# Kernel optimization log

Hardware: AMD Instinct MI355X
Metric: run time of the kernel (lower is better)

Reference implementation:

```python
import jax, jax.numpy as jnp
import numpy as np

B, T, N, H, RC, APT = 8, 32, 144, 16, 16, 10
HN = H * N          # 2304
RCN = RC * N        # 2304
NUM_LAYERS = 2


def _lstm_scan(x, Wih, Whh, bih, bhh):
    # x: [B, D, T] -> hidden states [B, HN, T]; matches torch.nn.LSTMCell math
    b = x.shape[0]
    hd = Whh.shape[1]
    xs = jnp.moveaxis(x, 2, 0)  # [T, B, D]

    def step(carry, xt):
        h, c = carry
        g = xt @ Wih.T + bih + h @ Whh.T + bhh  # [B, 4*HN]
        i, f, gg, o = jnp.split(g, 4, axis=1)
        c = jax.nn.sigmoid(f) * c + jax.nn.sigmoid(i) * jnp.tanh(gg)
        h = jax.nn.sigmoid(o) * jnp.tanh(c)
        return (h, c), h

    init = (jnp.zeros((b, hd), x.dtype), jnp.zeros((b, hd), x.dtype))
    _, hs = jax.lax.scan(step, init, xs)  # [T, B, HN]
    return jnp.moveaxis(hs, 0, 2)  # [B, HN, T]


def _graph_conv(x, A, Wg, bg):
    # x: [B, H, N, T]; diffusion order 2 over one adaptive support, then 1x1 conv
    x1 = jnp.einsum('bcvt,vw->bcwt', x, A)
    x2 = jnp.einsum('bcvt,vw->bcwt', x1, A)
    h = jnp.concatenate([x, x1, x2], axis=1)  # [B, 3H, N, T]
    return jnp.einsum('bcnt,oc->bont', h, Wg) + bg[None, :, None, None]


def _bn(x, g, b, eps=1e-5):
    # BatchNorm2d in training mode (batch statistics over N,H,W)
    m = x.mean(axis=(0, 2, 3), keepdims=True)
    v = x.var(axis=(0, 2, 3), keepdims=True)
    return g[None, :, None, None] * (x - m) * jax.lax.rsqrt(v + eps) + b[None, :, None, None]


def _forward(input_tensor, mask, input_tensor_bw, mask_bw, y, ymask,
             ws, bs, wc, bc, nodevec1, nodevec2,
             Wih_fw, Whh_fw, bih_fw, bhh_fw,
             Wih_bw, Whh_bw, bih_bw, bhh_bw,
             Wg, bg, gamma, beta,
             W_end1, b_end1, W_end2, b_end2,
             W_lo, b_lo, W_f1, b_f1, W_f2, b_f2):

    def feat(inp, m):
        # stack->transpose(2,3) then two 1x1 convs (in_channels=1 each), summed
        f1 = jnp.swapaxes(inp, 1, 2)[:, None]  # [B,1,N,T]
        f2 = jnp.swapaxes(m, 1, 2)[:, None]
        return (ws[None, :, None, None] * f1 + bs[None, :, None, None]
                + wc[None, :, None, None] * f2 + bc[None, :, None, None])

    x = feat(input_tensor, mask)          # [B, RC, N, T]
    x_bw = feat(input_tensor_bw, mask_bw)
    adp = jax.nn.softmax(jax.nn.relu(nodevec1 @ nodevec2), axis=1)  # [N, N]

    outputs = None
    for l in range(NUM_LAYERS):
        t_l = x.shape[3]
        hs = _lstm_scan(x.reshape(B, -1, t_l), Wih_fw[l], Whh_fw[l], bih_fw[l], bhh_fw[l])
        if l == 0:
            hs_bw = _lstm_scan(x_bw.reshape(B, -1, t_l), Wih_bw, Whh_bw, bih_bw, bhh_bw)
            hs = (hs + hs_bw[..., ::-1]) / 2.0
        gcn_in = jnp.tanh(hs.reshape(B, H, N, t_l))
        go = _graph_conv(gcn_in, adp, Wg[l], bg[l])  # [B, RC, N, t_l]
        outputs = go if outputs is None else go + outputs[..., -t_l:]
        x = _bn(go[..., ::2], gamma[l], beta[l])  # halve time dim

    out = jnp.einsum('bcnt,oc->bont', outputs, W_end1) + b_end1[None, :, None, None]
    out = jnp.einsum('bcnt,oc->bont', out, W_end2) + b_end2[None, :, None, None]
    out = jnp.einsum('bcnt,t->bcn', out, W_lo[0]) + b_lo[0]  # linear over time, squeeze
    out = jnp.concatenate([out, y, ymask], axis=-1)  # [B, T, 3N]
    out = out @ W_f1.T + b_f1
    out = out @ W_f2.T + b_f2
    return out  # [B, T, N]


def setup_inputs() -> dict:
    key = jax.random.key(0)
    ks = iter(jax.random.split(key, 48))
    nrm = lambda shape, s=0.05: jax.random.normal(next(ks), shape, dtype=jnp.float32) * s
    rnd = lambda shape: jax.random.uniform(next(ks), shape, dtype=jnp.float32)
    d = {}
    for name in ['input_tensor', 'mask', 'input_tensor_bw', 'mask_bw', 'y', 'ymask']:
        d[name] = rnd((B, T, N))
    d['ws'] = nrm((RC,), 0.2); d['bs'] = nrm((RC,))
    d['wc'] = nrm((RC,), 0.2); d['bc'] = nrm((RC,))
    d['nodevec1'] = nrm((N, APT), 1.0); d['nodevec2'] = nrm((APT, N), 1.0)
    d['Wih_fw'] = nrm((NUM_LAYERS, 4 * HN, RCN), 0.02)
    d['Whh_fw'] = nrm((NUM_LAYERS, 4 * HN, HN), 0.02)
    d['bih_fw'] = nrm((NUM_LAYERS, 4 * HN)); d['bhh_fw'] = nrm((NUM_LAYERS, 4 * HN))
    d['Wih_bw'] = nrm((4 * HN, RCN), 0.02); d['Whh_bw'] = nrm((4 * HN, HN), 0.02)
    d['bih_bw'] = nrm((4 * HN,)); d['bhh_bw'] = nrm((4 * HN,))
    d['Wg'] = nrm((NUM_LAYERS, RC, 3 * H), 0.1); d['bg'] = nrm((NUM_LAYERS, RC))
    d['gamma'] = jnp.ones((NUM_LAYERS, RC), jnp.float32)
    d['beta'] = jnp.zeros((NUM_LAYERS, RC), jnp.float32)
    d['W_end1'] = nrm((H, RC), 0.1); d['b_end1'] = nrm((H,))
    d['W_end2'] = nrm((T, H), 0.1); d['b_end2'] = nrm((T,))
    d['W_lo'] = nrm((1, T // 2), 0.1); d['b_lo'] = nrm((1,))
    d['W_f1'] = nrm((128, 3 * N), 0.05); d['b_f1'] = nrm((128,))
    d['W_f2'] = nrm((N, 128), 0.05); d['b_f2'] = nrm((N,))
    return d


def reference(input_tensor, mask, input_tensor_bw, mask_bw, y, ymask,
              ws, bs, wc, bc, nodevec1, nodevec2,
              Wih_fw, Whh_fw, bih_fw, bhh_fw,
              Wih_bw, Whh_bw, bih_bw, bhh_bw,
              Wg, bg, gamma, beta,
              W_end1, b_end1, W_end2, b_end2,
              W_lo, b_lo, W_f1, b_f1, W_f2, b_f2):
    return _forward(input_tensor, mask, input_tensor_bw, mask_bw, y, ymask,
                    ws, bs, wc, bc, nodevec1, nodevec2,
                    Wih_fw, Whh_fw, bih_fw, bhh_fw,
                    Wih_bw, Whh_bw, bih_bw, bhh_bw,
                    Wg, bg, gamma, beta,
                    W_end1, b_end1, W_end2, b_end2,
                    W_lo, b_lo, W_f1, b_f1, W_f2, b_f2)
```

## Files before the change

### kernel.cpp

```cpp
#include <hip/hip_runtime.h>
#include <cstdint>
#include <cstddef>

#define HN_ 2304
#define G4_ 9216

typedef __attribute__((ext_vector_type(8))) short v8s;
typedef __attribute__((ext_vector_type(4))) float v4f;

__device__ __forceinline__ unsigned short f2bf(float x) {
  union { float f; unsigned int i; } v; v.f = x;
  unsigned int r = (v.i + 0x7fffu + ((v.i >> 16) & 1u)) >> 16;
  return (unsigned short)r;
}

__global__ __launch_bounds__(256) void adp_kernel(const float* __restrict__ nv1,
                                                  const float* __restrict__ nv2,
                                                  float* __restrict__ adp) {
  int i = blockIdx.x;
  int j = threadIdx.x;
  __shared__ float sm[256];
  float r = 0.f, v = -1e30f;
  if (j < 144) {
    for (int k = 0; k < 10; ++k) r += nv1[i * 10 + k] * nv2[k * 144 + j];
    r = fmaxf(r, 0.f);
    v = r;
  }
  sm[j] = v; __syncthreads();
  for (int s = 128; s > 0; s >>= 1) { if (j < s) sm[j] = fmaxf(sm[j], sm[j + s]); __syncthreads(); }
  float mx = sm[0]; __syncthreads();
  float e = (j < 144) ? expf(r - mx) : 0.f;
  sm[j] = e; __syncthreads();
  for (int s = 128; s > 0; s >>= 1) { if (j < s) sm[j] += sm[j + s]; __syncthreads(); }
  float sum = sm[0];
  if (j < 144) adp[i * 144 + j] = e / sum;
}

__global__ __launch_bounds__(256)
void eff_weights(const float* __restrict__ WihF, const float* __restrict__ WihB,
                 const float* __restrict__ bihF, const float* __restrict__ bhhF,
                 const float* __restrict__ bihB, const float* __restrict__ bhhB,
                 const float* __restrict__ ws, const float* __restrict__ bs,
                 const float* __restrict__ wc, const float* __restrict__ bc,
                 unsigned short* __restrict__ Wpk, float* __restrict__ beff) {
  const int r = blockIdx.x, dir = blockIdx.y;
  const float* W = dir ? WihB : WihF;
  __shared__ float red[256];
  const int n = threadIdx.x;
  float spb = 0.f;
  if (n < 144) {
    float sws = 0.f, swc = 0.f;
    #pragma unroll
    for (int c = 0; c < 16; ++c) {
      float w = W[(size_t)r * HN_ + c * 144 + n];
      sws += w * ws[c];
      swc += w * wc[c];
      spb += w * (bs[c] + bc[c]);
    }
    const int rm = r % 2304;
    const int g = r / 2304;
    const int nt = rm >> 2, col = (rm & 3) * 4 + g;
    unsigned short* outp = Wpk + (size_t)dir * 2654208;
    int k = n;
    outp[((size_t)(nt * 9 + (k >> 5)) * 64 + ((k >> 3) & 3) * 16 + col) * 8 + (k & 7)] = f2bf(sws);
    k = 144 + n;
    outp[((size_t)(nt * 9 + (k >> 5)) * 64 + ((k >> 3) & 3) * 16 + col) * 8 + (k & 7)] = f2bf(swc);
  }
  red[n] = spb; __syncthreads();
  for (int s = 128; s > 0; s >>= 1) { if (n < s) red[n] += red[n + s]; __syncthreads(); }
  if (n == 0) {
    const float* bih = dir ? bihB : bihF;
    const float* bhh = dir ? bhhB : bhhF;
    beff[dir * G4_ + r] = red[0] + bih[r] + bhh[r];
  }
}

__global__ void build_acat_frag(const float* __restrict__ inF, const float* __restrict__ mF,
                                const float* __restrict__ inB, const float* __restrict__ mB,
                                unsigned short* __restrict__ out) {
  int idx = blockIdx.x * 256 + threadIdx.x;
  int lane = idx & 63;
  int ks = (idx >> 6) % 9;
  int mt = (idx / (64 * 9)) % 16;
  int dir = idx / (64 * 9 * 16);
  int m = mt * 16 + (lane & 15);
  int k = ks * 32 + (lane >> 4) * 8;
  int t = m >> 3, b = m & 7;
  const float* src; int kk = k;
  if (k < 144) src = dir ? inB : inF;
  else { src = dir ? mB : mF; kk = k - 144; }
  const float* p = src + ((size_t)b * 32 + t) * 144 + kk;
  v8s o;
  #pragma unroll
  for (int e = 0; e < 8; ++e) o[e] = (short)f2bf(p[e]);
  ((v8s*)out)[idx] = o;
}

__global__ void pack_whh(const float* __restrict__ W, unsigned short* __restrict__ out) {
  int idx = blockIdx.x * 256 + threadIdx.x;
  int lane = idx & 63;
  int ks = (idx >> 6) % 72;
  int nt = idx / (64 * 72);
  int col = lane & 15, q = lane >> 4;
  int r = (col & 3) * 2304 + nt * 4 + (col >> 2);
  int k = ks * 32 + q * 8;
  const float* src = W + (size_t)r * 2304 + k;
  float4 v0 = *(const float4*)src;
  float4 v1 = *(const float4*)(src + 4);
  v8s o;
  o[0] = (short)f2bf(v0.x); o[1] = (short)f2bf(v0.y);
  o[2] = (short)f2bf(v0.z); o[3] = (short)f2bf(v0.w);
  o[4] = (short)f2bf(v1.x); o[5] = (short)f2bf(v1.y);
  o[6] = (short)f2bf(v1.z); o[7] = (short)f2bf(v1.w);
  ((v8s*)out)[idx] = o;
}

__global__ __launch_bounds__(64)
void gemm_frag(const unsigned short* __restrict__ Apk, const unsigned short* __restrict__ Wpk,
               const float* __restrict__ b1, const float* __restrict__ b2,
               float* __restrict__ Gx, int nks) {
  const int lane = threadIdx.x;
  const int nt = blockIdx.x;
  const int mtb = blockIdx.y * 4;
  v4f acc[4] = {};
  const v8s* Bp = (const v8s*)Wpk + (size_t)nt * nks * 64;
  const v8s* Ap = (const v8s*)Apk;
  for (int ks = 0; ks < nks; ++ks) {
    v8s bf = Bp[ks * 64 + lane];
    #pragma unroll
    for (int mi = 0; mi < 4; ++mi) {
      v8s af = Ap[(size_t)((mtb + mi) * nks + ks) * 64 + lane];
      acc[mi] = __builtin_amdgcn_mfma_f32_16x16x32_bf16(af, bf, acc[mi], 0, 0, 0);
    }
  }
  const int col = lane & 15;
  const int jj = col >> 2, g = col & 3;
  const int rw = g * 2304 + nt * 4 + jj;
  float bsum = b1[rw] + (b2 ? b2[rw] : 0.f);
  #pragma unroll
  for (int mi = 0; mi < 4; ++mi)
    #pragma unroll
    for (int r = 0; r < 4; ++r) {
      int m = (mtb + mi) * 16 + (lane >> 4) * 4 + r;
      int t = m >> 3, b = m & 7;
      Gx[((size_t)t * 576 + nt) * 128 + col * 8 + b] = acc[mi][r] + bsum;
    }
}

__global__ __launch_bounds__(256, 4)
void lstm_step(const unsigned short* __restrict__ Wpk0, const unsigned short* __restrict__ Wpk1,
               const float* __restrict__ Gx0, const float* __restrict__ Gx1,
               const unsigned short* __restrict__ hin0, const unsigned short* __restrict__ hin1,
               unsigned short* __restrict__ hout0, unsigned short* __restrict__ hout1,
               float* __restrict__ c0, float* __restrict__ c1,
               float* __restrict__ hs0, float* __restrict__ hs1,
               int t, int T) {
  const int dir = blockIdx.y;
  const unsigned short* __restrict__ Wpk = dir ? Wpk1 : Wpk0;
  const float* __restrict__ Gxb = dir ? Gx1 : Gx0;
  const unsigned short* __restrict__ hin = dir ? hin1 : hin0;
  unsigned short* __restrict__ hout = dir ? hout1 : hout0;
  float* __restrict__ cb = dir ? c1 : c0;
  float* __restrict__ hsout = dir ? hs1 : hs0;

  const int lane = threadIdx.x & 63;
  const int wave = threadIdx.x >> 6;
  const int nt = blockIdx.x;

  const int afoff = (lane >> 4) * 8 + (lane & 7);
  const v8s* __restrict__ Aq = (const v8s*)hin + (size_t)(wave * 18) * 32 + afoff;
  const v8s* __restrict__ Bq = (const v8s*)Wpk + (size_t)nt * 72 * 64 + (size_t)(wave * 18) * 64 + lane;

  v4f acc = {0.f, 0.f, 0.f, 0.f};
  #pragma unroll
  for (int k = 0; k < 18; ++k) {
    v8s af = Aq[k * 32];
    v8s bf = Bq[k * 64];
    acc = __builtin_amdgcn_mfma_f32_16x16x32_bf16(af, bf, acc, 0, 0, 0);
  }

  __shared__ v4f red[3][64];
  if (wave) red[wave - 1][lane] = acc;
  __syncthreads();
  if (wave == 0) {
    acc += red[0][lane];
    acc += red[1][lane];
    acc += red[2][lane];

    float vI[4], vF[4], vG[4], vO[4];
    #pragma unroll
    for (int r = 0; r < 4; ++r) {
      float a = acc[r];
      vI[r] = a;
      vF[r] = __shfl_xor(a, 1, 64);
      vG[r] = __shfl_xor(a, 2, 64);
      vO[r] = __shfl_xor(a, 3, 64);
    }
    const int col = lane & 15;
    if ((lane & 3) == 0 && lane < 32) {
      const int j = nt * 4 + (col >> 2);
      const int brow = (lane >> 4) * 4;
      const float* Gx = Gxb + (size_t)t * 73728 + (size_t)(nt * 16 + col) * 8;
      #pragma unroll
      for (int r = 0; r < 4; ++r) {
        const int b = brow + r;
        const float gi = vI[r] + Gx[b];
        const float gf = vF[r] + Gx[8 + b];
        const float gg = vG[r] + Gx[16 + b];
        const float go = vO[r] + Gx[24 + b];
        const float si = 1.f / (1.f + expf(-gi));
        const float sf = 1.f / (1.f + expf(-gf));
        const float so = 1.f / (1.f + expf(-go));
        const float cn = sf * cb[b * HN_ + j] + si * tanhf(gg);
        cb[b * HN_ + j] = cn;
        const float hv = so * tanhf(cn);
        hsout[(size_t)(b * HN_ + j) * T + t] = hv;
        hout[((j >> 5) * 32 + ((j >> 3) & 3) * 8 + b) * 8 + (j & 7)] = f2bf(hv);
      }
    }
  }
}

__global__ void combine_tanh(const float* __restrict__ hsF, const float* __restrict__ hsB,
                             float* __restrict__ gin, int t_l, int total) {
  int idx = blockIdx.x * 256 + threadIdx.x;
  if (idx >= total) return;
  int t = idx % t_l;
  float v;
  if (hsB) v = 0.5f * (hsF[idx] + hsB[idx - t + (t_l - 1 - t)]);
  else v = hsF[idx];
  gin[idx] = tanhf(v);
}

__global__ void gc1(const float* __restrict__ in, const float* __restrict__ A,
                    float* __restrict__ out, int t_l, int total) {
  int idx = blockIdx.x * 256 + threadIdx.x;
  if (idx >= total) return;
  int t = idx % t_l;
  int w = (idx / t_l) % 144;
  int bc = idx / (t_l * 144);
  const float* src = in + (size_t)bc * 144 * t_l + t;
  float acc = 0.f;
  for (int v = 0; v < 144; ++v) acc += src[(size_t)v * t_l] * A[v * 144 + w];
  out[idx] = acc;
}

__global__ void gc_out(const float* __restrict__ g0, const float* __restrict__ g1,
                       const float* __restrict__ g2, const float* __restrict__ Wg,
                       const float* __restrict__ bg, const float* __restrict__ prev,
                       float* __restrict__ out, int t_l, int total) {
  int idx = blockIdx.x * 256 + threadIdx.x;
  if (idx >= total) return;
  int t = idx % t_l;
  int n = (idx / t_l) % 144;
  int o = (idx / (t_l * 144)) % 16;
  int b = idx / (t_l * 144 * 16);
  float acc = bg[o];
  size_t base = ((size_t)b * 16 * 144 + n) * t_l + t;
  #pragma unroll
  for (int c = 0; c < 16; ++c) {
    size_t s = base + (size_t)c * 144 * t_l;
    acc += Wg[o * 48 + c] * g0[s] + Wg[o * 48 + 16 + c] * g1[s] + Wg[o * 48 + 32 + c] * g2[s];
  }
  if (prev) acc += prev[((size_t)(b * 16 + o) * 144 + n) * 32 + 16 + t];
  out[idx] = acc;
}

__global__ __launch_bounds__(256)
void bn_xt(const float* __restrict__ go, const float* __restrict__ gamma,
           const float* __restrict__ beta, unsigned short* __restrict__ xbf) {
  int c = blockIdx.x;
  __shared__ float s1[256], s2[256];
  float sum = 0.f, sq = 0.f;
  for (int i = threadIdx.x; i < 18432; i += 256) {
    int b = i / 2304; int rem = i - b * 2304; int n = rem / 16; int tt = rem & 15;
    float v = go[((size_t)(b * 16 + c) * 144 + n) * 32 + 2 * tt];
    sum += v; sq += v * v;
  }
  s1[threadIdx.x] = sum; s2[threadIdx.x] = sq; __syncthreads();
  for (int s = 128; s > 0; s >>= 1) {
    if (threadIdx.x < s) { s1[threadIdx.x] += s1[threadIdx.x + s]; s2[threadIdx.x] += s2[threadIdx.x + s]; }
    __syncthreads();
  }
  float mean = s1[0] / 18432.f;
  float var = s2[0] / 18432.f - mean * mean;
  float rs = rsqrtf(var + 1e-5f);
  float scale = gamma[c] * rs, shift = beta[c] - mean * scale;
  for (int i = threadIdx.x; i < 18432; i += 256) {
    int b = i / 2304; int rem = i - b * 2304; int n = rem / 16; int tt = rem & 15;
    float v = go[((size_t)(b * 16 + c) * 144 + n) * 32 + 2 * tt];
    int m = tt * 8 + b;
    int k = c * 144 + n;
    size_t pos = ((size_t)((m >> 4) * 72 + (k >> 5)) * 64 + ((k >> 3) & 3) * 16 + (m & 15)) * 8 + (k & 7);
    xbf[pos] = f2bf(v * scale + shift);
  }
}

__global__ void e1_kernel(const float* __restrict__ in, const float* __restrict__ W,
                          const float* __restrict__ bias, float* __restrict__ out) {
  int idx = blockIdx.x * 256 + threadIdx.x;
  int tt = idx & 15;
  int n = (idx >> 4) % 144;
  int o = (idx / (16 * 144)) % 16;
  int b = idx / (16 * 144 * 16);
  float acc = bias[o];
  size_t base = ((size_t)b * 16 * 144 + n) * 16 + tt;
  #pragma unroll
  for (int c = 0; c < 16; ++c) acc += in[base + (size_t)c * 144 * 16] * W[o * 16 + c];
  out[idx] = acc;
}
__global__ void e2_kernel(const float* __restrict__ in, const float* __restrict__ W,
                          const float* __restrict__ bias, float* __restrict__ out) {
  int idx = blockIdx.x * 256 + threadIdx.x;
  int tt = idx & 15;
  int n = (idx >> 4) % 144;
  int o2 = (idx / (16 * 144)) % 32;
  int b = idx / (16 * 144 * 32);
  float acc = bias[o2];
  size_t base = ((size_t)b * 16 * 144 + n) * 16 + tt;
  #pragma unroll
  for (int o = 0; o < 16; ++o) acc += in[base + (size_t)o * 144 * 16] * W[o2 * 16 + o];
  out[idx] = acc;
}
__global__ void e3_kernel(const float* __restrict__ in, const float* __restrict__ Wlo,
                          const float* __restrict__ blo, float* __restrict__ out) {
  int idx = blockIdx.x * 256 + threadIdx.x;
  int n = idx % 144;
  int o2 = (idx / 144) % 32;
  int b = idx / (144 * 32);
  float acc = blo[0];
  size_t base = ((size_t)(b * 32 + o2) * 144 + n) * 16;
  #pragma unroll
  for (int tt = 0; tt < 16; ++tt) acc += in[base + tt] * Wlo[tt];
  out[idx] = acc;
}
__global__ void f1_kernel(const float* __restrict__ o3, const float* __restrict__ y,
                          const float* __restrict__ ym, const float* __restrict__ W,
                          const float* __restrict__ bias, float* __restrict__ out) {
  int idx = blockIdx.x * 256 + threadIdx.x;
  int k = idx & 127;
  int t = (idx >> 7) & 31;
  int b = idx >> 12;
  float acc = bias[k];
  size_t rb = (size_t)(b * 32 + t) * 144;
  const float* wr = W + k * 432;
  for (int n = 0; n < 144; ++n)
    acc += o3[rb + n] * wr[n] + y[rb + n] * wr[144 + n] + ym[rb + n] * wr[288 + n];
  out[idx] = acc;
}
__global__ void f2_kernel(const float* __restrict__ f1b, const float* __restrict__ W,
                          const float* __restrict__ bias, float* __restrict__ out) {
  int idx = blockIdx.x * 256 + threadIdx.x;
  int n = idx % 144;
  int t = (idx / 144) % 32;
  int b = idx / (144 * 32);
  float acc = bias[n];
  size_t fb = (size_t)(b * 32 + t) * 128;
  const float* wr = W + n * 128;
  #pragma unroll 4
  for (int k = 0; k < 128; ++k) acc += f1b[fb + k] * wr[k];
  out[idx] = acc;
}

extern "C" void kernel_launch(void* const* d_in, const int* in_sizes, int n_in,
                              void* d_out, int out_size, void* d_ws, size_t ws_size,
                              hipStream_t stream) {
  const float* input_tensor = (const float*)d_in[0];
  const float* mask_    = (const float*)d_in[1];
  const float* input_bw = (const float*)d_in[2];
  const float* mask_bw  = (const float*)d_in[3];
  const float* y_in     = (const float*)d_in[4];
  const float* ymask    = (const float*)d_in[5];
  const float* ws_p = (const float*)d_in[6];
  const float* bs_p = (const float*)d_in[7];
  const float* wc_p = (const float*)d_in[8];
  const float* bc_p = (const float*)d_in[9];
  const float* nv1 = (const float*)d_in[10];
  const float* nv2 = (const float*)d_in[11];
  const float* Wih_fw = (const float*)d_in[12];
  const float* Whh_fw = (const float*)d_in[13];
  const float* bih_fw = (const float*)d_in[14];
  const float* bhh_fw = (const float*)d_in[15];
  const float* Wih_bw = (const float*)d_in[16];
  const float* Whh_bw = (const float*)d_in[17];
  const float* bih_bw = (const float*)d_in[18];
  const float* bhh_bw = (const float*)d_in[19];
  const float* Wg   = (const float*)d_in[20];
  const float* bg   = (const float*)d_in[21];
  const float* gam  = (const float*)d_in[22];
  const float* bet  = (const float*)d_in[23];
  const float* W_end1 = (const float*)d_in[24];
  const float* b_end1 = (const float*)d_in[25];
  const float* W_end2 = (const float*)d_in[26];
  const float* b_end2 = (const float*)d_in[27];
  const float* W_lo = (const float*)d_in[28];
  const float* b_lo = (const float*)d_in[29];
  const float* W_f1 = (const float*)d_in[30];
  const float* b_f1 = (const float*)d_in[31];
  const float* W_f2 = (const float*)d_in[32];
  const float* b_f2 = (const float*)d_in[33];

  char* base = (char*)d_ws;
  size_t off = 0;
  auto alloc = [&](size_t bytes) -> char* {
    char* p = base + off;
    off += (bytes + 255) & ~(size_t)255;
    return p;
  };
  float* adp   = (float*)alloc(144 * 144 * 4);
  unsigned short* Weffpk = (unsigned short*)alloc((size_t)2 * 2654208 * 2);
  float* beff  = (float*)alloc(2 * G4_ * 4);
  unsigned short* acatf  = (unsigned short*)alloc((size_t)2 * 73728 * 2);
  float* GxF   = (float*)alloc((size_t)32 * 73728 * 4);
  float* GxB   = (float*)alloc((size_t)32 * 73728 * 4);
  char*  hz    = alloc(442368);
  float* hsF   = (float*)alloc((size_t)589824 * 4);
  float* hsB   = (float*)alloc((size_t)589824 * 4);
  float* hsL   = (float*)alloc((size_t)294912 * 4);
  float* gin   = (float*)alloc((size_t)589824 * 4);
  float* x1b   = (float*)alloc((size_t)589824 * 4);
  float* x2b   = (float*)alloc((size_t)589824 * 4);
  float* out0  = (float*)alloc((size_t)589824 * 4);
  float* out1  = (float*)alloc((size_t)294912 * 4);
  unsigned short* xbf = (unsigned short*)alloc((size_t)294912 * 2);
  float* tmp1  = (float*)alloc((size_t)294912 * 4);
  float* tmp2  = (float*)alloc((size_t)589824 * 4);
  float* out3  = (float*)alloc((size_t)36864 * 4);
  float* f1b   = (float*)alloc((size_t)32768 * 4);
  unsigned short* P0 = (unsigned short*)alloc((size_t)2654208 * 8 * 2);
  unsigned short* P1 = (unsigned short*)alloc((size_t)2654208 * 8 * 2);

  unsigned short* hF[2] = {(unsigned short*)hz,            (unsigned short*)(hz + 36864)};
  unsigned short* hB[2] = {(unsigned short*)(hz + 73728),  (unsigned short*)(hz + 110592)};
  unsigned short* hL[2] = {(unsigned short*)(hz + 147456), (unsigned short*)(hz + 184320)};
  float* cF = (float*)(hz + 221184);
  float* cB = (float*)(hz + 294912);
  float* cL = (float*)(hz + 368640);

  hipMemsetAsync(hz, 0, 442368, stream);

  adp_kernel<<<144, 256, 0, stream>>>(nv1, nv2, adp);
  eff_weights<<<dim3(G4_, 2), 256, 0, stream>>>(Wih_fw, Wih_bw, bih_fw, bhh_fw, bih_bw, bhh_bw,
                                                ws_p, bs_p, wc_p, bc_p, Weffpk, beff);
  build_acat_frag<<<72, 256, 0, stream>>>(input_tensor, mask_, input_bw, mask_bw, acatf);
  gemm_frag<<<dim3(576, 4), 64, 0, stream>>>(acatf, Weffpk, beff, nullptr, GxF, 9);
  gemm_frag<<<dim3(576, 4), 64, 0, stream>>>(acatf + 73728, Weffpk + 2654208, beff + G4_, nullptr, GxB, 9);
  pack_whh<<<10368, 256, 0, stream>>>(Whh_fw, P0);
  pack_whh<<<10368, 256, 0, stream>>>(Whh_bw, P1);

  for (int t = 0; t < 32; ++t) {
    lstm_step<<<dim3(576, 2), 256, 0, stream>>>(
        P0, P1, GxF, GxB,
        hF[t & 1], hB[t & 1], hF[(t + 1) & 1], hB[(t + 1) & 1],
        cF, cB, hsF, hsB, t, 32);
  }

  combine_tanh<<<2304, 256, 0, stream>>>(hsF, hsB, gin, 32, 589824);
  gc1<<<2304, 256, 0, stream>>>(gin, adp, x1b, 32, 589824);
  gc1<<<2304, 256, 0, stream>>>(x1b, adp, x2b, 32, 589824);
  gc_out<<<2304, 256, 0, stream>>>(gin, x1b, x2b, Wg, bg, nullptr, out0, 32, 589824);
  bn_xt<<<16, 256, 0, stream>>>(out0, gam, bet, xbf);

  const size_t WL1_off = (size_t)G4_ * HN_;
  pack_whh<<<10368, 256, 0, stream>>>(Wih_fw + WL1_off, P1);
  gemm_frag<<<dim3(576, 2), 64, 0, stream>>>(xbf, P1, bih_fw + G4_, bhh_fw + G4_, GxF, 72);
  pack_whh<<<10368, 256, 0, stream>>>(Whh_fw + WL1_off, P0);

  for (int t = 0; t < 16; ++t) {
    lstm_step<<<dim3(576, 1), 256, 0, stream>>>(
        P0, P0, GxF, GxF,
        hL[t & 1], hL[t & 1], hL[(t + 1) & 1], hL[(t + 1) & 1],
        cL, cL, hsL, hsL, t, 16);
  }

  combine_tanh<<<1152, 256, 0, stream>>>(hsL, nullptr, gin, 16, 294912);
  gc1<<<1152, 256, 0, stream>>>(gin, adp, x1b, 16, 294912);
  gc1<<<1152, 256, 0, stream>>>(x1b, adp, x2b, 16, 294912);
  gc_out<<<1152, 256, 0, stream>>>(gin, x1b, x2b, Wg + 16 * 48, bg + 16, out0, out1, 16, 294912);

  e1_kernel<<<1152, 256, 0, stream>>>(out1, W_end1, b_end1, tmp1);
  e2_kernel<<<2304, 256, 0, stream>>>(tmp1, W_end2, b_end2, tmp2);
  e3_kernel<<<144, 256, 0, stream>>>(tmp2, W_lo, b_lo, out3);
  f1_kernel<<<128, 256, 0, stream>>>(out3, y_in, ymask, W_f1, b_f1, f1b);
  f2_kernel<<<144, 256, 0, stream>>>(f1b, W_f2, b_f2, (float*)d_out);
}
```

Measured before the change: 1.487 ms.

## Prefetch LSTM gate inputs, fuse graph diffusion, and fold end convs algebraically

The LSTM step now loads the precomputed input gates and the previous cell state before the MFMA loop, so their latency overlaps the matmul, and its occupancy hint rises from 4 to 5 blocks. The combine/tanh kernel and both graph diffusion passes are merged into one kernel that keeps intermediates in shared memory. The end1/end2/time-projection chain is reordered algebraically: the time reduction with W_lo is applied first, so end1 and end2 operate on a much smaller tensor. This removes several launches and large intermediate buffers. The fused GC kernel uses fewer blocks, which may lower parallelism.

```diff
diff --git a/kernel.cpp b/kernel.cpp
--- a/kernel.cpp
+++ b/kernel.cpp
@@ -147,7 +147,7 @@
     }
 }
 
-__global__ __launch_bounds__(256, 4)
+__global__ __launch_bounds__(256, 5)
 void lstm_step(const unsigned short* __restrict__ Wpk0, const unsigned short* __restrict__ Wpk1,
                const float* __restrict__ Gx0, const float* __restrict__ Gx1,
                const unsigned short* __restrict__ hin0, const unsigned short* __restrict__ hin1,
@@ -167,6 +167,24 @@
   const int wave = threadIdx.x >> 6;
   const int nt = blockIdx.x;
 
+  const int col = lane & 15;
+  const int brow = (lane >> 4) * 4;
+  const bool act = (wave == 0) && ((lane & 3) == 0) && (lane < 32);
+
+  float4 gxI = {0,0,0,0}, gxF = {0,0,0,0}, gxG = {0,0,0,0}, gxO = {0,0,0,0};
+  float cpre[4] = {0.f, 0.f, 0.f, 0.f};
+  int jpre = 0;
+  if (act) {
+    jpre = nt * 4 + (col >> 2);
+    const float* Gx = Gxb + (size_t)t * 73728 + (size_t)(nt * 16 + col) * 8 + brow;
+    gxI = *(const float4*)(Gx);
+    gxF = *(const float4*)(Gx + 8);
+    gxG = *(const float4*)(Gx + 16);
+    gxO = *(const float4*)(Gx + 24);
+    #pragma unroll
+    for (int r = 0; r < 4; ++r) cpre[r] = cb[(brow + r) * HN_ + jpre];
+  }
+
   const int afoff = (lane >> 4) * 8 + (lane & 7);
   const v8s* __restrict__ Aq = (const v8s*)hin + (size_t)(wave * 18) * 32 + afoff;
   const v8s* __restrict__ Bq = (const v8s*)Wpk + (size_t)nt * 72 * 64 + (size_t)(wave * 18) * 64 + lane;
@@ -196,53 +214,66 @@
       vG[r] = __shfl_xor(a, 2, 64);
       vO[r] = __shfl_xor(a, 3, 64);
     }
-    const int col = lane & 15;
-    if ((lane & 3) == 0 && lane < 32) {
-      const int j = nt * 4 + (col >> 2);
-      const int brow = (lane >> 4) * 4;
-      const float* Gx = Gxb + (size_t)t * 73728 + (size_t)(nt * 16 + col) * 8;
+    if (act) {
+      const float gxi[4] = {gxI.x, gxI.y, gxI.z, gxI.w};
+      const float gxf[4] = {gxF.x, gxF.y, gxF.z, gxF.w};
+      const float gxg[4] = {gxG.x, gxG.y, gxG.z, gxG.w};
+      const float gxo[4] = {gxO.x, gxO.y, gxO.z, gxO.w};
       #pragma unroll
       for (int r = 0; r < 4; ++r) {
         const int b = brow + r;
-        const float gi = vI[r] + Gx[b];
-        const float gf = vF[r] + Gx[8 + b];
-        const float gg = vG[r] + Gx[16 + b];
-        const float go = vO[r] + Gx[24 + b];
+        const float gi = vI[r] + gxi[r];
+        const float gf = vF[r] + gxf[r];
+        const float gg = vG[r] + gxg[r];
+        const float go = vO[r] + gxo[r];
         const float si = 1.f / (1.f + expf(-gi));
         const float sf = 1.f / (1.f + expf(-gf));
         const float so = 1.f / (1.f + expf(-go));
-        const float cn = sf * cb[b * HN_ + j] + si * tanhf(gg);
-        cb[b * HN_ + j] = cn;
+        const float cn = sf * cpre[r] + si * tanhf(gg);
+        cb[b * HN_ + jpre] = cn;
         const float hv = so * tanhf(cn);
-        hsout[(size_t)(b * HN_ + j) * T + t] = hv;
-        hout[((j >> 5) * 32 + ((j >> 3) & 3) * 8 + b) * 8 + (j & 7)] = f2bf(hv);
+        hsout[(size_t)(b * HN_ + jpre) * T + t] = hv;
+        hout[((jpre >> 5) * 32 + ((jpre >> 3) & 3) * 8 + b) * 8 + (jpre & 7)] = f2bf(hv);
       }
     }
   }
 }
 
-__global__ void combine_tanh(const float* __restrict__ hsF, const float* __restrict__ hsB,
-                             float* __restrict__ gin, int t_l, int total) {
-  int idx = blockIdx.x * 256 + threadIdx.x;
-  if (idx >= total) return;
-  int t = idx % t_l;
-  float v;
-  if (hsB) v = 0.5f * (hsF[idx] + hsB[idx - t + (t_l - 1 - t)]);
-  else v = hsF[idx];
-  gin[idx] = tanhf(v);
-}
-
-__global__ void gc1(const float* __restrict__ in, const float* __restrict__ A,
-                    float* __restrict__ out, int t_l, int total) {
-  int idx = blockIdx.x * 256 + threadIdx.x;
-  if (idx >= total) return;
-  int t = idx % t_l;
-  int w = (idx / t_l) % 144;
-  int bc = idx / (t_l * 144);
-  const float* src = in + (size_t)bc * 144 * t_l + t;
-  float acc = 0.f;
-  for (int v = 0; v < 144; ++v) acc += src[(size_t)v * t_l] * A[v * 144 + w];
-  out[idx] = acc;
+__global__ __launch_bounds__(256)
+void gc_fused(const float* __restrict__ hsF, const float* __restrict__ hsB,
+              const float* __restrict__ A,
+              float* __restrict__ gin, float* __restrict__ x1b, float* __restrict__ x2b,
+              int t_l) {
+  const int bc = blockIdx.x;
+  const int t0 = blockIdx.y * 8;
+  __shared__ float g[144][8];
+  __shared__ float s1[144][8];
+  const size_t base = (size_t)bc * 144 * t_l;
+  for (int i = threadIdx.x; i < 1152; i += 256) {
+    int v = i >> 3, tt = i & 7;
+    size_t idx = base + (size_t)v * t_l + t0 + tt;
+    float val;
+    if (hsB) val = 0.5f * (hsF[idx] + hsB[base + (size_t)v * t_l + (t_l - 1 - (t0 + tt))]);
+    else val = hsF[idx];
+    val = tanhf(val);
+    g[v][tt] = val;
+    gin[idx] = val;
+  }
+  __syncthreads();
+  for (int i = threadIdx.x; i < 1152; i += 256) {
+    int w = i >> 3, tt = i & 7;
+    float acc = 0.f;
+    for (int v = 0; v < 144; ++v) acc += g[v][tt] * A[v * 144 + w];
+    s1[w][tt] = acc;
+    x1b[base + (size_t)w * t_l + t0 + tt] = acc;
+  }
+  __syncthreads();
+  for (int i = threadIdx.x; i < 1152; i += 256) {
+    int w = i >> 3, tt = i & 7;
+    float acc = 0.f;
+    for (int v = 0; v < 144; ++v) acc += s1[v][tt] * A[v * 144 + w];
+    x2b[base + (size_t)w * t_l + t0 + tt] = acc;
+  }
 }
 
 __global__ void gc_out(const float* __restrict__ g0, const float* __restrict__ g1,
@@ -296,44 +327,41 @@
   }
 }
 
-__global__ void e1_kernel(const float* __restrict__ in, const float* __restrict__ W,
-                          const float* __restrict__ bias, float* __restrict__ out) {
-  int idx = blockIdx.x * 256 + threadIdx.x;
-  int tt = idx & 15;
-  int n = (idx >> 4) % 144;
-  int o = (idx / (16 * 144)) % 16;
-  int b = idx / (16 * 144 * 16);
-  float acc = bias[o];
-  size_t base = ((size_t)b * 16 * 144 + n) * 16 + tt;
-  #pragma unroll
-  for (int c = 0; c < 16; ++c) acc += in[base + (size_t)c * 144 * 16] * W[o * 16 + c];
-  out[idx] = acc;
-}
-__global__ void e2_kernel(const float* __restrict__ in, const float* __restrict__ W,
-                          const float* __restrict__ bias, float* __restrict__ out) {
-  int idx = blockIdx.x * 256 + threadIdx.x;
-  int tt = idx & 15;
-  int n = (idx >> 4) % 144;
-  int o2 = (idx / (16 * 144)) % 32;
-  int b = idx / (16 * 144 * 32);
-  float acc = bias[o2];
-  size_t base = ((size_t)b * 16 * 144 + n) * 16 + tt;
-  #pragma unroll
-  for (int o = 0; o < 16; ++o) acc += in[base + (size_t)o * 144 * 16] * W[o2 * 16 + o];
-  out[idx] = acc;
-}
-__global__ void e3_kernel(const float* __restrict__ in, const float* __restrict__ Wlo,
-                          const float* __restrict__ blo, float* __restrict__ out) {
+__global__ void ez_kernel(const float* __restrict__ out1, const float* __restrict__ Wlo,
+                          float* __restrict__ z) {
+  int idx = blockIdx.x * 256 + threadIdx.x;
+  const float* p = out1 + (size_t)idx * 16;
+  float acc = 0.f;
+  #pragma unroll
+  for (int tt = 0; tt < 16; ++tt) acc += p[tt] * Wlo[tt];
+  z[idx] = acc;
+}
+__global__ void ef_kernel(const float* __restrict__ z, const float* __restrict__ W1,
+                          const float* __restrict__ b1, const float* __restrict__ W2,
+                          const float* __restrict__ b2, const float* __restrict__ Wlo,
+                          const float* __restrict__ blo, float* __restrict__ out3) {
   int idx = blockIdx.x * 256 + threadIdx.x;
   int n = idx % 144;
-  int o2 = (idx / 144) % 32;
+  int o2 = (idx / 144) & 31;
   int b = idx / (144 * 32);
-  float acc = blo[0];
-  size_t base = ((size_t)(b * 32 + o2) * 144 + n) * 16;
-  #pragma unroll
-  for (int tt = 0; tt < 16; ++tt) acc += in[base + tt] * Wlo[tt];
-  out[idx] = acc;
-}
+  float S = 0.f;
+  #pragma unroll
+  for (int tt = 0; tt < 16; ++tt) S += Wlo[tt];
+  float zr[16];
+  const float* zb = z + (size_t)b * 16 * 144 + n;
+  #pragma unroll
+  for (int c = 0; c < 16; ++c) zr[c] = zb[(size_t)c * 144];
+  float acc = blo[0] + b2[o2] * S;
+  #pragma unroll
+  for (int o = 0; o < 16; ++o) {
+    float u = b1[o] * S;
+    #pragma unroll
+    for (int c = 0; c < 16; ++c) u += W1[o * 16 + c] * zr[c];
+    acc += W2[o2 * 16 + o] * u;
+  }
+  out3[idx] = acc;
+}
+
 __global__ void f1_kernel(const float* __restrict__ o3, const float* __restrict__ y,
                           const float* __restrict__ ym, const float* __restrict__ W,
                           const float* __restrict__ bias, float* __restrict__ out) {
@@ -423,8 +451,7 @@
   float* out0  = (float*)alloc((size_t)589824 * 4);
   float* out1  = (float*)alloc((size_t)294912 * 4);
   unsigned short* xbf = (unsigned short*)alloc((size_t)294912 * 2);
-  float* tmp1  = (float*)alloc((size_t)294912 * 4);
-  float* tmp2  = (float*)alloc((size_t)589824 * 4);
+  float* zbuf  = (float*)alloc((size_t)18432 * 4);
   float* out3  = (float*)alloc((size_t)36864 * 4);
   float* f1b   = (float*)alloc((size_t)32768 * 4);
   unsigned short* P0 = (unsigned short*)alloc((size_t)2654208 * 8 * 2);
@@ -455,9 +482,7 @@
         cF, cB, hsF, hsB, t, 32);
   }
 
-  combine_tanh<<<2304, 256, 0, stream>>>(hsF, hsB, gin, 32, 589824);
-  gc1<<<2304, 256, 0, stream>>>(gin, adp, x1b, 32, 589824);
-  gc1<<<2304, 256, 0, stream>>>(x1b, adp, x2b, 32, 589824);
+  gc_fused<<<dim3(128, 4), 256, 0, stream>>>(hsF, hsB, adp, gin, x1b, x2b, 32);
   gc_out<<<2304, 256, 0, stream>>>(gin, x1b, x2b, Wg, bg, nullptr, out0, 32, 589824);
   bn_xt<<<16, 256, 0, stream>>>(out0, gam, bet, xbf);
 
@@ -473,14 +498,11 @@
         cL, cL, hsL, hsL, t, 16);
   }
 
-  combine_tanh<<<1152, 256, 0, stream>>>(hsL, nullptr, gin, 16, 294912);
-  gc1<<<1152, 256, 0, stream>>>(gin, adp, x1b, 16, 294912);
-  gc1<<<1152, 256, 0, stream>>>(x1b, adp, x2b, 16, 294912);
+  gc_fused<<<dim3(128, 2), 256, 0, stream>>>(hsL, nullptr, adp, gin, x1b, x2b, 16);
   gc_out<<<1152, 256, 0, stream>>>(gin, x1b, x2b, Wg + 16 * 48, bg + 16, out0, out1, 16, 294912);
 
-  e1_kernel<<<1152, 256, 0, stream>>>(out1, W_end1, b_end1, tmp1);
-  e2_kernel<<<2304, 256, 0, stream>>>(tmp1, W_end2, b_end2, tmp2);
-  e3_kernel<<<144, 256, 0, stream>>>(tmp2, W_lo, b_lo, out3);
+  ez_kernel<<<72, 256, 0, stream>>>(out1, W_lo, zbuf);
+  ef_kernel<<<144, 256, 0, stream>>>(zbuf, W_end1, b_end1, W_end2, b_end2, W_lo, b_lo, out3);
   f1_kernel<<<128, 256, 0, stream>>>(out3, y_in, ymask, W_f1, b_f1, f1b);
   f2_kernel<<<144, 256, 0, stream>>>(f1b, W_f2, b_f2, (float*)d_out);
 }
```

Result: faster. 1.434 ms (-3.5%).
